# Kernel optimization log

Measured on AMD Instinct MI355X. Metric: run time of the kernel, lower is better.

## Reference

```python
import jax, jax.numpy as jnp
import numpy as np

GROUPS = 8
NUM_HEADS = 4
EPS = 1e-5

def setup_inputs() -> dict:
    key = jax.random.key(0)
    k1, k2, k3 = jax.random.split(key, 3)
    B, C, H, W = 4, 128, 64, 64
    x = jax.random.normal(k1, (B, C, H, W), dtype=jnp.float32)
    gn_w = jnp.ones((C,), jnp.float32)
    gn_b = jnp.zeros((C,), jnp.float32)
    qkv_w = jax.random.normal(k2, (3 * C, C), dtype=jnp.float32) * (1.0 / np.sqrt(C))
    qkv_b = jnp.zeros((3 * C,), jnp.float32)
    proj_w = jax.random.normal(k3, (C, C), dtype=jnp.float32) * (1.0 / np.sqrt(C))
    proj_b = jnp.zeros((C,), jnp.float32)
    return {"x": x, "gn_w": gn_w, "gn_b": gn_b, "qkv_w": qkv_w,
            "qkv_b": qkv_b, "proj_w": proj_w, "proj_b": proj_b}

def group_norm(x, w, b):
    B, C, H, W = x.shape
    xg = x.reshape(B, GROUPS, C // GROUPS, H, W)
    mean = jnp.mean(xg, axis=(2, 3, 4), keepdims=True)
    var = jnp.var(xg, axis=(2, 3, 4), keepdims=True)
    xn = ((xg - mean) * jax.lax.rsqrt(var + EPS)).reshape(B, C, H, W)
    return xn * w[None, :, None, None] + b[None, :, None, None]

def reference(x, gn_w, gn_b, qkv_w, qkv_b, proj_w, proj_b):
    B, C, H, W = x.shape
    nh = NUM_HEADS
    hd = C // nh
    xn = group_norm(x, gn_w, gn_b)  # residual is the NORMALIZED x (torch code reassigns x)
    # 1x1 conv == channel matmul
    qkv = jnp.einsum('oc,bchw->bohw', qkv_w, xn) + qkv_b[None, :, None, None]
    qkv = qkv.reshape(B, 3, nh, hd, H * W)
    q, k, v = qkv[:, 0], qkv[:, 1], qkv[:, 2]          # [B, nh, hd, HW]
    attn = jnp.einsum('bhcd,bhce->bhde', q, k) * (C ** -0.5)  # note: full-C scale, as in torch code
    attn = jax.nn.softmax(attn, axis=-1)
    out = jnp.einsum('bhde,bhce->bhcd', attn, v).reshape(B, C, H, W)
    out = jnp.einsum('oc,bchw->bohw', proj_w, out) + proj_b[None, :, None, None]
    return out + xn
```

## Files before the change

kernel.cpp:

```cpp
#include <hip/hip_runtime.h>
#include <math.h>

#define BATCH 4
#define C 128
#define HW 4096
#define G 8
#define CPG 16
#define NH 4
#define HD 32
#define EPS 1e-5f
#define SCALE 0.08838834764831845f
#define LOG2E 1.44269504088896340f

typedef unsigned int uint;
typedef unsigned short ushort;
typedef __attribute__((ext_vector_type(8))) short bf16x8;
typedef __attribute__((ext_vector_type(4))) float f32x4;

__device__ __forceinline__ ushort f2bf(float x) {
  uint u = __float_as_uint(x);
  u += 0x7fff + ((u >> 16) & 1);
  return (ushort)(u >> 16);
}
__device__ __forceinline__ ushort f2bf_r(float x) {
  return (ushort)((__float_as_uint(x) + 0x8000u) >> 16);
}
__device__ __forceinline__ float bf2f(ushort h) {
  return __uint_as_float(((uint)h) << 16);
}
__device__ __forceinline__ uint pk(float a, float b) {
  uint ua = __float_as_uint(a) + 0x8000u;
  uint ub = __float_as_uint(b) + 0x8000u;
  return __builtin_amdgcn_perm(ub, ua, 0x07060302);
}
__device__ __forceinline__ bf16x8 as_bf(uint4 u) {
  union { uint4 a; bf16x8 b; } x; x.a = u; return x.b;
}
__device__ __forceinline__ float fexp2(float x) {
#if __has_builtin(__builtin_amdgcn_exp2f)
  return __builtin_amdgcn_exp2f(x);
#else
  return __exp2f(x);
#endif
}

__global__ __launch_bounds__(256) void gn_part(
    const float* __restrict__ x, float* __restrict__ stats) {
  const int bg = blockIdx.x >> 3, chunk = blockIdx.x & 7;
  const float* xp = x + (size_t)bg * (CPG * HW) + chunk * 8192;
  const int tid = threadIdx.x;
  float s = 0.f, ss = 0.f;
  #pragma unroll
  for (int j = 0; j < 8; j++) {
    float4 v = ((const float4*)xp)[j * 256 + tid];
    s += (v.x + v.y) + (v.z + v.w);
    ss += (v.x * v.x + v.y * v.y) + (v.z * v.z + v.w * v.w);
  }
  #pragma unroll
  for (int off = 32; off; off >>= 1) {
    s  += __shfl_down(s, off);
    ss += __shfl_down(ss, off);
  }
  __shared__ float rs[4], rss[4];
  const int lane = tid & 63, wid = tid >> 6;
  if (lane == 0) { rs[wid] = s; rss[wid] = ss; }
  __syncthreads();
  if (tid == 0) {
    stats[(bg * 8 + chunk) * 2]     = (rs[0] + rs[1]) + (rs[2] + rs[3]);
    stats[(bg * 8 + chunk) * 2 + 1] = (rss[0] + rss[1]) + (rss[2] + rss[3]);
  }
}

__global__ __launch_bounds__(256) void gn_apply(
    const float* __restrict__ x, const float* __restrict__ w,
    const float* __restrict__ b, const float* __restrict__ stats,
    ushort* __restrict__ xnb) {
  const int c = blockIdx.x, batch = blockIdx.y;
  const int bg = batch * G + (c >> 4);
  float s = 0.f, ss = 0.f;
  #pragma unroll
  for (int k = 0; k < 8; k++) {
    s  += stats[(bg * 8 + k) * 2];
    ss += stats[(bg * 8 + k) * 2 + 1];
  }
  const float mean = s * (1.0f / 65536.0f);
  const float var  = ss * (1.0f / 65536.0f) - mean * mean;
  const float inv  = rsqrtf(var + EPS);
  const float ca = w[c] * inv;
  const float cb = b[c] - mean * ca;
  const size_t base = ((size_t)batch * C + c) * HW;
  const float* xp = x + base;
  ushort* op = xnb + base;
  const int tid = threadIdx.x;
  #pragma unroll
  for (int j = 0; j < 4; j++) {
    int i = (j * 256 + tid) * 4;
    float4 v = *(const float4*)&xp[i];
    uint2 u;
    u.x = pk(fmaf(v.x, ca, cb), fmaf(v.y, ca, cb));
    u.y = pk(fmaf(v.z, ca, cb), fmaf(v.w, ca, cb));
    *(uint2*)&op[i] = u;
  }
}

__global__ __launch_bounds__(256) void qkv_gemm(
    const ushort* __restrict__ xnb, const float* __restrict__ w,
    const float* __restrict__ bias, ushort* __restrict__ qkvb) {
  const int b = blockIdx.z, m0 = blockIdx.y * 64, n0 = blockIdx.x * 64;
  const int tid = threadIdx.x, lane = tid & 63, wv = tid >> 6;
  const int li = lane & 15, g = lane >> 4;
  __shared__ ushort Ws[64][40];
  __shared__ ushort Xs[64][40];

  f32x4 acc[4];
  #pragma unroll
  for (int nt = 0; nt < 4; nt++) acc[nt] = (f32x4){0.f, 0.f, 0.f, 0.f};

  const int oW = tid >> 2, cW0 = (tid & 3) * 8;
  const int nX = tid & 63, cX0 = (tid >> 6) * 8;

  for (int k0 = 0; k0 < C; k0 += 32) {
    __syncthreads();
    float4 wa = *(const float4*)&w[(size_t)(m0 + oW) * C + k0 + cW0];
    float4 wb = *(const float4*)&w[(size_t)(m0 + oW) * C + k0 + cW0 + 4];
    uint4 uw = {pk(wa.x, wa.y), pk(wa.z, wa.w), pk(wb.x, wb.y), pk(wb.z, wb.w)};
    *(uint4*)&Ws[oW][cW0] = uw;
    ushort tx[8];
    #pragma unroll
    for (int j = 0; j < 8; j++)
      tx[j] = xnb[(size_t)(b * C + k0 + cX0 + j) * HW + n0 + nX];
    uint4 ux;
    ux.x = tx[0] | ((uint)tx[1] << 16);
    ux.y = tx[2] | ((uint)tx[3] << 16);
    ux.z = tx[4] | ((uint)tx[5] << 16);
    ux.w = tx[6] | ((uint)tx[7] << 16);
    *(uint4*)&Xs[nX][cX0] = ux;
    __syncthreads();

    bf16x8 af = *(const bf16x8*)&Ws[wv * 16 + li][g * 8];
    #pragma unroll
    for (int nt = 0; nt < 4; nt++) {
      bf16x8 bfr = *(const bf16x8*)&Xs[nt * 16 + li][g * 8];
      acc[nt] = __builtin_amdgcn_mfma_f32_16x16x32_bf16(af, bfr, acc[nt], 0, 0, 0);
    }
  }
  const int ob = m0 + wv * 16 + g * 4;
  #pragma unroll
  for (int r = 0; r < 4; r++) {
    float bi = bias[ob + r];
    #pragma unroll
    for (int nt = 0; nt < 4; nt++) {
      qkvb[(size_t)(b * 3 * C + ob + r) * HW + n0 + nt * 16 + li] = f2bf(acc[nt][r] + bi);
    }
  }
}

__global__ __launch_bounds__(256) void kvprep_kernel(
    const ushort* __restrict__ qkvb, ushort* __restrict__ kt) {
  const int bh = blockIdx.y, b = bh >> 2, h = bh & 3;
  const int e0 = blockIdx.x * 64;
  const ushort* kp = qkvb + (size_t)(b * 3 * C + C + h * HD) * HW;
  ushort* ktp = kt + (size_t)bh * HW * HD;
  const int t = threadIdx.x;

  __shared__ ushort Kt[32][66];
  {
    const int c = t >> 3, e8 = (t & 7) * 8;
    *(uint4*)&Kt[c][e8] = *(const uint4*)&kp[(size_t)c * HW + e0 + e8];
  }
  __syncthreads();
  {
    const int e = t >> 2, c0 = (t & 3) * 8;
    ushort o[8];
    #pragma unroll
    for (int j = 0; j < 8; j++) o[j] = Kt[c0 + j][e];
    uint4 u;
    u.x = o[0] | ((uint)o[1] << 16);
    u.y = o[2] | ((uint)o[3] << 16);
    u.z = o[4] | ((uint)o[5] << 16);
    u.w = o[6] | ((uint)o[7] << 16);
    *(uint4*)&ktp[(size_t)(e0 + e) * HD + c0] = u;
  }
}

__global__ __launch_bounds__(512, 4) void attn_kernel(
    ushort* __restrict__ qkv, const ushort* __restrict__ kt) {
  const int bh = blockIdx.y, b = bh >> 2, h = bh & 3;
  const int tid = threadIdx.x, lane = tid & 63, wv = tid >> 6;
  const int li = lane & 15, g = lane >> 4;
  const int grp = wv >> 2, w4 = wv & 3;
  ushort* qp = qkv + (size_t)(b * 3 * C + h * HD) * HW;
  const ushort* vpl = qkv + (size_t)(b * 3 * C + 2 * C + h * HD) * HW;
  const ushort* ktp = kt + (size_t)bh * HW * HD;
  const int d0 = blockIdx.x * 128 + w4 * 32;

  __shared__ ushort Ks[2][2][32][40];
  __shared__ ushort Vs[2][2][32][40];
  __shared__ float OP[8][64][19];

  const float qs = SCALE * LOG2E;
  bf16x8 qf[2];
  #pragma unroll
  for (int dt = 0; dt < 2; dt++) {
    int d = d0 + dt * 16 + li;
    float qv[8];
    #pragma unroll
    for (int j = 0; j < 8; j++)
      qv[j] = bf2f(qp[(size_t)(g * 8 + j) * HW + d]) * qs;
    uint4 qu = {pk(qv[0], qv[1]), pk(qv[2], qv[3]), pk(qv[4], qv[5]), pk(qv[6], qv[7])};
    qf[dt] = as_bf(qu);
  }

  f32x4 O[2][2];
  #pragma unroll
  for (int dt = 0; dt < 2; dt++)
    #pragma unroll
    for (int ct = 0; ct < 2; ct++) O[dt][ct] = (f32x4){0.f, 0.f, 0.f, 0.f};
  f32x4 lacc[2] = {(f32x4){0.f, 0.f, 0.f, 0.f}, (f32x4){0.f, 0.f, 0.f, 0.f}};
  const uint one2 = 0x3F803F80u;
  const bf16x8 ones = as_bf((uint4){one2, one2, one2, one2});

  const int gt = tid & 255;
  const bool isK = gt < 128;
  const int t2 = gt & 127;
  const int srow = t2 >> 2, scol8 = (t2 & 3) * 8;
  const ushort* gK = ktp + (size_t)(grp * 64) * 1024 + t2 * 8;
  const ushort* gV = vpl + (size_t)srow * HW + grp * 2048 + scol8;

  uint4 st = isK ? *(const uint4*)&gK[0] : *(const uint4*)&gV[0];
  if (isK) *(uint4*)&Ks[grp][0][srow][scol8] = st;
  else     *(uint4*)&Vs[grp][0][srow][scol8] = st;
  st = isK ? *(const uint4*)&gK[1024] : *(const uint4*)&gV[32];
  __syncthreads();

  for (int it = 0; it < 64; it++) {
    const int cur = it & 1, nxt = cur ^ 1;
    if (isK) *(uint4*)&Ks[grp][nxt][srow][scol8] = st;
    else     *(uint4*)&Vs[grp][nxt][srow][scol8] = st;

    bf16x8 kf0 = *(const bf16x8*)&Ks[grp][cur][li][g * 8];
    bf16x8 kf1 = *(const bf16x8*)&Ks[grp][cur][16 + li][g * 8];
    uint2 va0 = *(const uint2*)&Vs[grp][cur][li][4 * g];
    uint2 va1 = *(const uint2*)&Vs[grp][cur][li][16 + 4 * g];
    uint2 vb0 = *(const uint2*)&Vs[grp][cur][16 + li][4 * g];
    uint2 vb1 = *(const uint2*)&Vs[grp][cur][16 + li][16 + 4 * g];
    bf16x8 vf0 = as_bf((uint4){va0.x, va0.y, va1.x, va1.y});
    bf16x8 vf1 = as_bf((uint4){vb0.x, vb0.y, vb1.x, vb1.y});

    const int tn = (it + 2) & 63;
    st = isK ? *(const uint4*)&gK[(size_t)tn * 1024] : *(const uint4*)&gV[tn * 32];

    const f32x4 z = (f32x4){0.f, 0.f, 0.f, 0.f};
    #pragma unroll
    for (int dt = 0; dt < 2; dt++) {
      f32x4 s0 = __builtin_amdgcn_mfma_f32_16x16x32_bf16(kf0, qf[dt], z, 0, 0, 0);
      f32x4 s1 = __builtin_amdgcn_mfma_f32_16x16x32_bf16(kf1, qf[dt], z, 0, 0, 0);
      float p0 = fexp2(s0[0]), p1 = fexp2(s0[1]), p2 = fexp2(s0[2]), p3 = fexp2(s0[3]);
      float p4 = fexp2(s1[0]), p5 = fexp2(s1[1]), p6 = fexp2(s1[2]), p7 = fexp2(s1[3]);
      uint4 pu = {pk(p0, p1), pk(p2, p3), pk(p4, p5), pk(p6, p7)};
      bf16x8 pf = as_bf(pu);
      lacc[dt] = __builtin_amdgcn_mfma_f32_16x16x32_bf16(ones, pf, lacc[dt], 0, 0, 0);
      O[dt][0] = __builtin_amdgcn_mfma_f32_16x16x32_bf16(vf0, pf, O[dt][0], 0, 0, 0);
      O[dt][1] = __builtin_amdgcn_mfma_f32_16x16x32_bf16(vf1, pf, O[dt][1], 0, 0, 0);
    }
    __syncthreads();
  }

  #pragma unroll
  for (int dt = 0; dt < 2; dt++) {
    #pragma unroll
    for (int ct = 0; ct < 2; ct++)
      #pragma unroll
      for (int r = 0; r < 4; r++) OP[wv][lane][dt * 8 + ct * 4 + r] = O[dt][ct][r];
    OP[wv][lane][16 + dt] = lacc[dt][0];
  }
  __syncthreads();
  const int pw = wv ^ 4;
  #pragma unroll
  for (int dt = 0; dt < 2; dt++) {
    const float inv = 1.0f / (lacc[dt][0] + OP[pw][lane][16 + dt]);
    const int d = d0 + dt * 16 + li;
    #pragma unroll
    for (int r = 0; r < 4; r++) {
      float val = O[dt][grp][r] + OP[pw][lane][dt * 8 + grp * 4 + r];
      qp[(size_t)(grp * 16 + g * 4 + r) * HW + d] = f2bf_r(val * inv);
    }
  }
}

__global__ __launch_bounds__(256) void proj_gemm(
    const ushort* __restrict__ qkvb, const float* __restrict__ w,
    const float* __restrict__ bias, const ushort* __restrict__ xnb, float* __restrict__ out) {
  const int b = blockIdx.z, m0 = blockIdx.y * 64, n0 = blockIdx.x * 64;
  const int tid = threadIdx.x, lane = tid & 63, wv = tid >> 6;
  const int li = lane & 15, g = lane >> 4;
  __shared__ ushort Ws[64][40];
  __shared__ ushort Xs[64][40];

  f32x4 acc[4];
  #pragma unroll
  for (int nt = 0; nt < 4; nt++) acc[nt] = (f32x4){0.f, 0.f, 0.f, 0.f};

  const int oW = tid >> 2, cW0 = (tid & 3) * 8;
  const int nX = tid & 63, cX0 = (tid >> 6) * 8;

  for (int k0 = 0; k0 < C; k0 += 32) {
    __syncthreads();
    float4 wa = *(const float4*)&w[(size_t)(m0 + oW) * C + k0 + cW0];
    float4 wb = *(const float4*)&w[(size_t)(m0 + oW) * C + k0 + cW0 + 4];
    uint4 uw = {pk(wa.x, wa.y), pk(wa.z, wa.w), pk(wb.x, wb.y), pk(wb.z, wb.w)};
    *(uint4*)&Ws[oW][cW0] = uw;
    ushort tx[8];
    #pragma unroll
    for (int j = 0; j < 8; j++)
      tx[j] = qkvb[(size_t)(b * 3 * C + k0 + cX0 + j) * HW + n0 + nX];
    uint4 ux;
    ux.x = tx[0] | ((uint)tx[1] << 16);
    ux.y = tx[2] | ((uint)tx[3] << 16);
    ux.z = tx[4] | ((uint)tx[5] << 16);
    ux.w = tx[6] | ((uint)tx[7] << 16);
    *(uint4*)&Xs[nX][cX0] = ux;
    __syncthreads();

    bf16x8 af = *(const bf16x8*)&Ws[wv * 16 + li][g * 8];
    #pragma unroll
    for (int nt = 0; nt < 4; nt++) {
      bf16x8 bfr = *(const bf16x8*)&Xs[nt * 16 + li][g * 8];
      acc[nt] = __builtin_amdgcn_mfma_f32_16x16x32_bf16(af, bfr, acc[nt], 0, 0, 0);
    }
  }
  const int ob = m0 + wv * 16 + g * 4;
  #pragma unroll
  for (int r = 0; r < 4; r++) {
    float bi = bias[ob + r];
    #pragma unroll
    for (int nt = 0; nt < 4; nt++) {
      size_t idx = (size_t)(b * C + ob + r) * HW + n0 + nt * 16 + li;
      out[idx] = acc[nt][r] + bi + bf2f(xnb[idx]);
    }
  }
}

extern "C" void kernel_launch(void* const* d_in, const int* in_sizes, int n_in,
                              void* d_out, int out_size, void* d_ws, size_t ws_size,
                              hipStream_t stream) {
  const float* x     = (const float*)d_in[0];
  const float* gn_w  = (const float*)d_in[1];
  const float* gn_b  = (const float*)d_in[2];
  const float* qkv_w = (const float*)d_in[3];
  const float* qkv_b = (const float*)d_in[4];
  const float* pw    = (const float*)d_in[5];
  const float* pb    = (const float*)d_in[6];
  float* out = (float*)d_out;

  float*  stats = (float*)d_ws;
  ushort* xnb   = (ushort*)((char*)d_ws + 4096);
  ushort* qkvb  = xnb + (size_t)BATCH * C * HW;
  ushort* kt    = qkvb + (size_t)BATCH * 3 * C * HW;

  gn_part<<<dim3(256), dim3(256), 0, stream>>>(x, stats);
  gn_apply<<<dim3(C, BATCH), dim3(256), 0, stream>>>(x, gn_w, gn_b, stats, xnb);
  qkv_gemm<<<dim3(HW / 64, 6, BATCH), dim3(256), 0, stream>>>(xnb, qkv_w, qkv_b, qkvb);
  kvprep_kernel<<<dim3(HW / 64, BATCH * NH), dim3(256), 0, stream>>>(qkvb, kt);
  attn_kernel<<<dim3(HW / 128, BATCH * NH), dim3(512), 0, stream>>>(qkvb, kt);
  proj_gemm<<<dim3(HW / 64, 2, BATCH), dim3(256), 0, stream>>>(qkvb, pw, pb, xnb, out);
}
```

Before: 147.2 us.

## Load full K into LDS in GEMMs, overlay attention smem, raise occupancy

The QKV and projection GEMMs now stage the entire 128-wide reduction dimension into padded LDS in a single pass with one barrier, replacing the four-step loop that synchronised twice per step. The attention kernel pads its K/V tiles to a different stride, splits 16-byte LDS accesses into 8-byte pieces, and overlays the output-reduction buffer on the K/V buffers with a union to shrink LDS use. It also raises the launch-bounds occupancy hint from 4 to 8, which may force register spilling. The bf16 pack helper switches to a hardware convert builtin when available, which changes rounding from the old add-and-truncate.

```diff
diff --git a/kernel.cpp b/kernel.cpp
--- a/kernel.cpp
+++ b/kernel.cpp
@@ -11,6 +11,8 @@
 #define EPS 1e-5f
 #define SCALE 0.08838834764831845f
 #define LOG2E 1.44269504088896340f
+#define KP 44
+#define GP 136
 
 typedef unsigned int uint;
 typedef unsigned short ushort;
@@ -29,9 +31,16 @@
   return __uint_as_float(((uint)h) << 16);
 }
 __device__ __forceinline__ uint pk(float a, float b) {
+#if __has_builtin(__builtin_amdgcn_cvt_pk_bf16_f32)
+  auto r = __builtin_amdgcn_cvt_pk_bf16_f32(a, b);
+  union { decltype(r) v; uint u; } x;
+  x.v = r;
+  return x.u;
+#else
   uint ua = __float_as_uint(a) + 0x8000u;
   uint ub = __float_as_uint(b) + 0x8000u;
   return __builtin_amdgcn_perm(ub, ua, 0x07060302);
+#endif
 }
 __device__ __forceinline__ bf16x8 as_bf(uint4 u) {
   union { uint4 a; bf16x8 b; } x; x.a = u; return x.b;
@@ -109,38 +118,47 @@
   const int b = blockIdx.z, m0 = blockIdx.y * 64, n0 = blockIdx.x * 64;
   const int tid = threadIdx.x, lane = tid & 63, wv = tid >> 6;
   const int li = lane & 15, g = lane >> 4;
-  __shared__ ushort Ws[64][40];
-  __shared__ ushort Xs[64][40];
+  __shared__ ushort Ws[64][GP];
+  __shared__ ushort Xs[64][GP];
+
+  {
+    const int row = tid >> 2, c0 = (tid & 3) * 32;
+    const float* wr = w + (size_t)(m0 + row) * C + c0;
+    #pragma unroll
+    for (int k = 0; k < 4; k++) {
+      float4 f0 = ((const float4*)wr)[k * 2];
+      float4 f1 = ((const float4*)wr)[k * 2 + 1];
+      uint4 u = {pk(f0.x, f0.y), pk(f0.z, f0.w), pk(f1.x, f1.y), pk(f1.z, f1.w)};
+      *(uint4*)&Ws[row][c0 + k * 8] = u;
+    }
+  }
+  {
+    const int nX = tid & 63, c0 = (tid >> 6) * 32;
+    const ushort* xb = xnb + (size_t)(b * C + c0) * HW + n0 + nX;
+    #pragma unroll
+    for (int k = 0; k < 4; k++) {
+      ushort t8[8];
+      #pragma unroll
+      for (int j = 0; j < 8; j++) t8[j] = xb[(size_t)(k * 8 + j) * HW];
+      uint4 u;
+      u.x = t8[0] | ((uint)t8[1] << 16);
+      u.y = t8[2] | ((uint)t8[3] << 16);
+      u.z = t8[4] | ((uint)t8[5] << 16);
+      u.w = t8[6] | ((uint)t8[7] << 16);
+      *(uint4*)&Xs[nX][c0 + k * 8] = u;
+    }
+  }
+  __syncthreads();
 
   f32x4 acc[4];
   #pragma unroll
   for (int nt = 0; nt < 4; nt++) acc[nt] = (f32x4){0.f, 0.f, 0.f, 0.f};
-
-  const int oW = tid >> 2, cW0 = (tid & 3) * 8;
-  const int nX = tid & 63, cX0 = (tid >> 6) * 8;
-
-  for (int k0 = 0; k0 < C; k0 += 32) {
-    __syncthreads();
-    float4 wa = *(const float4*)&w[(size_t)(m0 + oW) * C + k0 + cW0];
-    float4 wb = *(const float4*)&w[(size_t)(m0 + oW) * C + k0 + cW0 + 4];
-    uint4 uw = {pk(wa.x, wa.y), pk(wa.z, wa.w), pk(wb.x, wb.y), pk(wb.z, wb.w)};
-    *(uint4*)&Ws[oW][cW0] = uw;
-    ushort tx[8];
-    #pragma unroll
-    for (int j = 0; j < 8; j++)
-      tx[j] = xnb[(size_t)(b * C + k0 + cX0 + j) * HW + n0 + nX];
-    uint4 ux;
-    ux.x = tx[0] | ((uint)tx[1] << 16);
-    ux.y = tx[2] | ((uint)tx[3] << 16);
-    ux.z = tx[4] | ((uint)tx[5] << 16);
-    ux.w = tx[6] | ((uint)tx[7] << 16);
-    *(uint4*)&Xs[nX][cX0] = ux;
-    __syncthreads();
-
-    bf16x8 af = *(const bf16x8*)&Ws[wv * 16 + li][g * 8];
+  #pragma unroll
+  for (int kk = 0; kk < 4; kk++) {
+    bf16x8 af = *(const bf16x8*)&Ws[wv * 16 + li][kk * 32 + g * 8];
     #pragma unroll
     for (int nt = 0; nt < 4; nt++) {
-      bf16x8 bfr = *(const bf16x8*)&Xs[nt * 16 + li][g * 8];
+      bf16x8 bfr = *(const bf16x8*)&Xs[nt * 16 + li][kk * 32 + g * 8];
       acc[nt] = __builtin_amdgcn_mfma_f32_16x16x32_bf16(af, bfr, acc[nt], 0, 0, 0);
     }
   }
@@ -183,7 +201,7 @@
   }
 }
 
-__global__ __launch_bounds__(512, 4) void attn_kernel(
+__global__ __launch_bounds__(512, 8) void attn_kernel(
     ushort* __restrict__ qkv, const ushort* __restrict__ kt) {
   const int bh = blockIdx.y, b = bh >> 2, h = bh & 3;
   const int tid = threadIdx.x, lane = tid & 63, wv = tid >> 6;
@@ -194,9 +212,13 @@
   const ushort* ktp = kt + (size_t)bh * HW * HD;
   const int d0 = blockIdx.x * 128 + w4 * 32;
 
-  __shared__ ushort Ks[2][2][32][40];
-  __shared__ ushort Vs[2][2][32][40];
-  __shared__ float OP[8][64][19];
+  struct SmemT {
+    union {
+      struct { ushort Ks[2][2][32][KP]; ushort Vs[2][2][32][KP]; } t;
+      float OP[8][64][19];
+    };
+  };
+  __shared__ SmemT sm;
 
   const float qs = SCALE * LOG2E;
   bf16x8 qf[2];
@@ -228,22 +250,36 @@
   const ushort* gV = vpl + (size_t)srow * HW + grp * 2048 + scol8;
 
   uint4 st = isK ? *(const uint4*)&gK[0] : *(const uint4*)&gV[0];
-  if (isK) *(uint4*)&Ks[grp][0][srow][scol8] = st;
-  else     *(uint4*)&Vs[grp][0][srow][scol8] = st;
+  if (isK) {
+    *(uint2*)&sm.t.Ks[grp][0][srow][scol8]     = (uint2){st.x, st.y};
+    *(uint2*)&sm.t.Ks[grp][0][srow][scol8 + 4] = (uint2){st.z, st.w};
+  } else {
+    *(uint2*)&sm.t.Vs[grp][0][srow][scol8]     = (uint2){st.x, st.y};
+    *(uint2*)&sm.t.Vs[grp][0][srow][scol8 + 4] = (uint2){st.z, st.w};
+  }
   st = isK ? *(const uint4*)&gK[1024] : *(const uint4*)&gV[32];
   __syncthreads();
 
   for (int it = 0; it < 64; it++) {
     const int cur = it & 1, nxt = cur ^ 1;
-    if (isK) *(uint4*)&Ks[grp][nxt][srow][scol8] = st;
-    else     *(uint4*)&Vs[grp][nxt][srow][scol8] = st;
-
-    bf16x8 kf0 = *(const bf16x8*)&Ks[grp][cur][li][g * 8];
-    bf16x8 kf1 = *(const bf16x8*)&Ks[grp][cur][16 + li][g * 8];
-    uint2 va0 = *(const uint2*)&Vs[grp][cur][li][4 * g];
-    uint2 va1 = *(const uint2*)&Vs[grp][cur][li][16 + 4 * g];
-    uint2 vb0 = *(const uint2*)&Vs[grp][cur][16 + li][4 * g];
-    uint2 vb1 = *(const uint2*)&Vs[grp][cur][16 + li][16 + 4 * g];
+    if (isK) {
+      *(uint2*)&sm.t.Ks[grp][nxt][srow][scol8]     = (uint2){st.x, st.y};
+      *(uint2*)&sm.t.Ks[grp][nxt][srow][scol8 + 4] = (uint2){st.z, st.w};
+    } else {
+      *(uint2*)&sm.t.Vs[grp][nxt][srow][scol8]     = (uint2){st.x, st.y};
+      *(uint2*)&sm.t.Vs[grp][nxt][srow][scol8 + 4] = (uint2){st.z, st.w};
+    }
+
+    uint2 ka0 = *(const uint2*)&sm.t.Ks[grp][cur][li][g * 8];
+    uint2 ka1 = *(const uint2*)&sm.t.Ks[grp][cur][li][g * 8 + 4];
+    uint2 kb0 = *(const uint2*)&sm.t.Ks[grp][cur][16 + li][g * 8];
+    uint2 kb1 = *(const uint2*)&sm.t.Ks[grp][cur][16 + li][g * 8 + 4];
+    bf16x8 kf0 = as_bf((uint4){ka0.x, ka0.y, ka1.x, ka1.y});
+    bf16x8 kf1 = as_bf((uint4){kb0.x, kb0.y, kb1.x, kb1.y});
+    uint2 va0 = *(const uint2*)&sm.t.Vs[grp][cur][li][4 * g];
+    uint2 va1 = *(const uint2*)&sm.t.Vs[grp][cur][li][16 + 4 * g];
+    uint2 vb0 = *(const uint2*)&sm.t.Vs[grp][cur][16 + li][4 * g];
+    uint2 vb1 = *(const uint2*)&sm.t.Vs[grp][cur][16 + li][16 + 4 * g];
     bf16x8 vf0 = as_bf((uint4){va0.x, va0.y, va1.x, va1.y});
     bf16x8 vf1 = as_bf((uint4){vb0.x, vb0.y, vb1.x, vb1.y});
 
@@ -271,18 +307,18 @@
     #pragma unroll
     for (int ct = 0; ct < 2; ct++)
       #pragma unroll
-      for (int r = 0; r < 4; r++) OP[wv][lane][dt * 8 + ct * 4 + r] = O[dt][ct][r];
-    OP[wv][lane][16 + dt] = lacc[dt][0];
+      for (int r = 0; r < 4; r++) sm.OP[wv][lane][dt * 8 + ct * 4 + r] = O[dt][ct][r];
+    sm.OP[wv][lane][16 + dt] = lacc[dt][0];
   }
   __syncthreads();
   const int pw = wv ^ 4;
   #pragma unroll
   for (int dt = 0; dt < 2; dt++) {
-    const float inv = 1.0f / (lacc[dt][0] + OP[pw][lane][16 + dt]);
+    const float inv = 1.0f / (lacc[dt][0] + sm.OP[pw][lane][16 + dt]);
     const int d = d0 + dt * 16 + li;
     #pragma unroll
     for (int r = 0; r < 4; r++) {
-      float val = O[dt][grp][r] + OP[pw][lane][dt * 8 + grp * 4 + r];
+      float val = O[dt][grp][r] + sm.OP[pw][lane][dt * 8 + grp * 4 + r];
       qp[(size_t)(grp * 16 + g * 4 + r) * HW + d] = f2bf_r(val * inv);
     }
   }
@@ -294,38 +330,47 @@
   const int b = blockIdx.z, m0 = blockIdx.y * 64, n0 = blockIdx.x * 64;
   const int tid = threadIdx.x, lane = tid & 63, wv = tid >> 6;
   const int li = lane & 15, g = lane >> 4;
-  __shared__ ushort Ws[64][40];
-  __shared__ ushort Xs[64][40];
+  __shared__ ushort Ws[64][GP];
+  __shared__ ushort Xs[64][GP];
+
+  {
+    const int row = tid >> 2, c0 = (tid & 3) * 32;
+    const float* wr = w + (size_t)(m0 + row) * C + c0;
+    #pragma unroll
+    for (int k = 0; k < 4; k++) {
+      float4 f0 = ((const float4*)wr)[k * 2];
+      float4 f1 = ((const float4*)wr)[k * 2 + 1];
+      uint4 u = {pk(f0.x, f0.y), pk(f0.z, f0.w), pk(f1.x, f1.y), pk(f1.z, f1.w)};
+      *(uint4*)&Ws[row][c0 + k * 8] = u;
+    }
+  }
+  {
+    const int nX = tid & 63, c0 = (tid >> 6) * 32;
+    const ushort* xb = qkvb + (size_t)(b * 3 * C + c0) * HW + n0 + nX;
+    #pragma unroll
+    for (int k = 0; k < 4; k++) {
+      ushort t8[8];
+      #pragma unroll
+      for (int j = 0; j < 8; j++) t8[j] = xb[(size_t)(k * 8 + j) * HW];
+      uint4 u;
+      u.x = t8[0] | ((uint)t8[1] << 16);
+      u.y = t8[2] | ((uint)t8[3] << 16);
+      u.z = t8[4] | ((uint)t8[5] << 16);
+      u.w = t8[6] | ((uint)t8[7] << 16);
+      *(uint4*)&Xs[nX][c0 + k * 8] = u;
+    }
+  }
+  __syncthreads();
 
   f32x4 acc[4];
   #pragma unroll
   for (int nt = 0; nt < 4; nt++) acc[nt] = (f32x4){0.f, 0.f, 0.f, 0.f};
-
-  const int oW = tid >> 2, cW0 = (tid & 3) * 8;
-  const int nX = tid & 63, cX0 = (tid >> 6) * 8;
-
-  for (int k0 = 0; k0 < C; k0 += 32) {
-    __syncthreads();
-    float4 wa = *(const float4*)&w[(size_t)(m0 + oW) * C + k0 + cW0];
-    float4 wb = *(const float4*)&w[(size_t)(m0 + oW) * C + k0 + cW0 + 4];
-    uint4 uw = {pk(wa.x, wa.y), pk(wa.z, wa.w), pk(wb.x, wb.y), pk(wb.z, wb.w)};
-    *(uint4*)&Ws[oW][cW0] = uw;
-    ushort tx[8];
-    #pragma unroll
-    for (int j = 0; j < 8; j++)
-      tx[j] = qkvb[(size_t)(b * 3 * C + k0 + cX0 + j) * HW + n0 + nX];
-    uint4 ux;
-    ux.x = tx[0] | ((uint)tx[1] << 16);
-    ux.y = tx[2] | ((uint)tx[3] << 16);
-    ux.z = tx[4] | ((uint)tx[5] << 16);
-    ux.w = tx[6] | ((uint)tx[7] << 16);
-    *(uint4*)&Xs[nX][cX0] = ux;
-    __syncthreads();
-
-    bf16x8 af = *(const bf16x8*)&Ws[wv * 16 + li][g * 8];
+  #pragma unroll
+  for (int kk = 0; kk < 4; kk++) {
+    bf16x8 af = *(const bf16x8*)&Ws[wv * 16 + li][kk * 32 + g * 8];
     #pragma unroll
     for (int nt = 0; nt < 4; nt++) {
-      bf16x8 bfr = *(const bf16x8*)&Xs[nt * 16 + li][g * 8];
+      bf16x8 bfr = *(const bf16x8*)&Xs[nt * 16 + li][kk * 32 + g * 8];
       acc[nt] = __builtin_amdgcn_mfma_f32_16x16x32_bf16(af, bfr, acc[nt], 0, 0, 0);
     }
   }
```

After: 170.9 us. 16.1% more time.
